# Kernel optimization log

Hardware: AMD Instinct MI355X
Metric: run time of the kernel (lower is better)

The kernel has to match this reference:

```python
import jax, jax.numpy as jnp
import numpy as np

T, D = 1024, 1024            # tokens, model dim
E, K = 16, 4                 # routed experts, top-k
G, TG = 4, 2                 # expert groups, limited (top) groups
INTER = 512                  # moe_inter_dim
SHARED_INTER = 2 * INTER     # n_shared_experts * moe_inter_dim
ROUTE_SCALE = 2.5
STD = 0.02


def setup_inputs() -> dict:
    key = jax.random.key(0)
    ks = jax.random.split(key, 9)
    return {
        "x": jax.random.normal(ks[0], (T, D), jnp.float32),
        "token_mask": jnp.ones((T,), jnp.bool_),
        "gate_w": jax.random.normal(ks[1], (E, D), jnp.float32) * STD,
        "gate_bias": jnp.zeros((E,), jnp.float32),  # e_score_correction_bias (zero-init)
        "gate_projs": jax.random.normal(ks[2], (E, INTER, D), jnp.float32) * STD,
        "up_projs": jax.random.normal(ks[3], (E, INTER, D), jnp.float32) * STD,
        "down_projs": jax.random.normal(ks[4], (E, D, INTER), jnp.float32) * STD,
        "shared_gate": jax.random.normal(ks[5], (SHARED_INTER, D), jnp.float32) * STD,
        "shared_up": jax.random.normal(ks[6], (SHARED_INTER, D), jnp.float32) * STD,
        "shared_down": jax.random.normal(ks[7], (D, SHARED_INTER), jnp.float32) * STD,
    }


def _route(x, gate_w, gate_bias):
    # sigmoid scoring with e_score_correction_bias + group-limited top-k (DeepSeek-V3 style)
    scores = jax.nn.sigmoid(x @ gate_w.T)                      # [T, E]
    s = (scores + gate_bias).reshape(T, G, E // G)             # bias-corrected, grouped
    group_scores = jax.lax.top_k(s, 2)[0].sum(-1)              # [T, G] sum of top-2 per group
    gidx = jax.lax.top_k(group_scores, TG)[1]                  # [T, TG]
    gmask = jax.nn.one_hot(gidx, G, dtype=s.dtype).sum(1)      # [T, G] selected-group mask
    masked = (s * gmask[:, :, None]).reshape(T, E)
    idx = jax.lax.top_k(masked, K)[1]                          # [T, K] expert indices
    w = jnp.take_along_axis(scores, idx, axis=1)               # gather original (unbiased) scores
    w = w / w.sum(-1, keepdims=True) * ROUTE_SCALE             # sigmoid renorm + route scale
    return w.astype(x.dtype), idx


def reference(x, token_mask, gate_w, gate_bias, gate_projs, up_projs,
              down_projs, shared_gate, shared_up, shared_down):
    w, idx = _route(x, gate_w, gate_bias)
    # dense combine weights [T, E]: combine[t, e] = sum_k w[t, k] * (idx[t, k] == e)
    combine = (jax.nn.one_hot(idx, E, dtype=x.dtype) * w[..., None]).sum(1)

    def body(acc, p):
        gp, up, dp, c = p                                      # per-expert SwiGLU
        inter = jax.nn.silu(x @ gp.T) * (x @ up.T)             # [T, INTER]
        return acc + c[:, None] * (inter @ dp.T), None

    routed, _ = jax.lax.scan(
        body, jnp.zeros_like(x), (gate_projs, up_projs, down_projs, combine.T))
    shared = (jax.nn.silu(x @ shared_gate.T) * (x @ shared_up.T)) @ shared_down.T
    return routed + shared
```

## Files before the change

### kernel.cpp

```cpp
#include <hip/hip_runtime.h>
#include <stdint.h>

#define TTOK 1024
#define DMODEL 1024
#define NEXP 16
#define TOPK 4
#define INTER 512
#define NSHI 1024
#define RSCALE 2.5f

typedef __bf16 bf16;
typedef __bf16 bf16x8 __attribute__((ext_vector_type(8)));
typedef __bf16 bf16x4 __attribute__((ext_vector_type(4)));
typedef float f32x4 __attribute__((ext_vector_type(4)));

#define APLANE 2064
#define BPLANE 1040

#define OFF_GP 0L
#define OFF_UP 8388608L
#define OFF_DP 16777216L
#define OFF_SG 25165824L
#define OFF_SU 26214400L
#define OFF_SD 27262976L
#define WTOT   28311552L

#define LGKM_BAR()                                            \
  do {                                                        \
    asm volatile("s_waitcnt lgkmcnt(0)" ::: "memory");        \
    __builtin_amdgcn_s_barrier();                             \
  } while (0)

__global__ __launch_bounds__(256)
void convert_kernel(const float* __restrict__ s0, const float* __restrict__ s1,
                    const float* __restrict__ s2, const float* __restrict__ s3,
                    const float* __restrict__ s4, const float* __restrict__ s5,
                    bf16* __restrict__ dst) {
  const long i = (long)blockIdx.x * 256 + threadIdx.x;
  const float* src;
  long local;
  if (i < 2097152)      { src = s0; local = i; }
  else if (i < 4194304) { src = s1; local = i - 2097152; }
  else if (i < 6291456) { src = s2; local = i - 4194304; }
  else if (i < 6553600) { src = s3; local = i - 6291456; }
  else if (i < 6815744) { src = s4; local = i - 6553600; }
  else                  { src = s5; local = i - 6815744; }
  const float4 v = ((const float4*)src)[local];
  bf16x4 o;
  o.x = (bf16)v.x; o.y = (bf16)v.y; o.z = (bf16)v.z; o.w = (bf16)v.w;
  ((bf16x4*)dst)[i] = o;
}

__global__ __launch_bounds__(256)
void scores_kernel(const float* __restrict__ x, const float* __restrict__ gw,
                   float* __restrict__ scores, bf16* __restrict__ xbf) {
  __shared__ float gws[16 * 1024];
  const int tid = threadIdx.x;
  const float4* gw4 = (const float4*)gw;
#pragma unroll
  for (int i0 = 0; i0 < 4096; i0 += 256) {
    const int i = i0 + tid;
    const int e = i >> 8;
    const int dq = (i & 255) << 2;
    const int dd = (dq + 4 * e) & 1023;
    ((float4*)gws)[(e << 8) + (dd >> 2)] = gw4[i];
  }
  {
    const long xb = (long)blockIdx.x * 1024;
#pragma unroll
    for (int p = 0; p < 4; ++p) {
      const long j = xb + p * 256 + tid;
      const float4 v = ((const float4*)x)[j];
      bf16x4 o;
      o.x = (bf16)v.x; o.y = (bf16)v.y; o.z = (bf16)v.z; o.w = (bf16)v.w;
      ((bf16x4*)xbf)[j] = o;
    }
  }
  __syncthreads();
  const int kq = tid >> 6;
  const int lane = tid & 63;
  const int tl = lane >> 4;
  const int e = lane & 15;
  const long token = (long)blockIdx.x * 4 + tl;
  float acc = 0.f;
  const int dbase = kq * 256;
#pragma unroll 8
  for (int i = 0; i < 256; i += 4) {
    const int d = dbase + i;
    const float4 xv = *(const float4*)&x[token * DMODEL + d];
    const float4 wv = *(const float4*)&gws[(e << 10) + ((d + 4 * e) & 1023)];
    acc += xv.x * wv.x + xv.y * wv.y + xv.z * wv.z + xv.w * wv.w;
  }
  __syncthreads();
  gws[kq * 64 + lane] = acc;
  __syncthreads();
  if (kq == 0) {
    const float s = gws[lane] + gws[64 + lane] + gws[128 + lane] + gws[192 + lane];
    scores[token * 16 + e] = s;
  }
}

__global__ __launch_bounds__(256)
void topk_kernel(const float* __restrict__ scores, const float* __restrict__ gb,
                 int* __restrict__ tokIdx, float* __restrict__ tokW,
                 int* __restrict__ counts) {
  __shared__ int h[NEXP];
  const int tid = threadIdx.x;
  if (tid < NEXP) h[tid] = 0;
  __syncthreads();
  const int t = blockIdx.x * 256 + tid;
  float sc[NEXP], s[NEXP];
#pragma unroll
  for (int e = 0; e < NEXP; ++e) {
    const float l = scores[t * NEXP + e];
    sc[e] = 1.f / (1.f + expf(-l));
    s[e] = sc[e] + gb[e];
  }
  float gsc[4];
#pragma unroll
  for (int g = 0; g < 4; ++g) {
    const float a = s[4 * g], b = s[4 * g + 1], c = s[4 * g + 2], d = s[4 * g + 3];
    gsc[g] = fmaxf(fmaxf(fmaxf(a + b, a + c), fmaxf(a + d, b + c)),
                   fmaxf(b + d, c + d));
  }
  int g0 = 0;
  for (int g = 1; g < 4; ++g) if (gsc[g] > gsc[g0]) g0 = g;
  int g1 = (g0 == 0) ? 1 : 0;
  for (int g = 0; g < 4; ++g) if (g != g0 && gsc[g] > gsc[g1]) g1 = g;
  float m[NEXP];
#pragma unroll
  for (int e = 0; e < NEXP; ++e) {
    const int g = e >> 2;
    m[e] = (g == g0 || g == g1) ? s[e] : -1.f;
  }
  int idx[TOPK]; float wv[TOPK]; float wsum = 0.f;
  for (int k = 0; k < TOPK; ++k) {
    int am = 0; float best = m[0];
    for (int e2 = 1; e2 < NEXP; ++e2)
      if (m[e2] > best) { best = m[e2]; am = e2; }
    idx[k] = am; wv[k] = sc[am]; wsum += sc[am]; m[am] = -2.f;
  }
  const float scl = RSCALE / wsum;
  for (int k = 0; k < TOPK; ++k) {
    tokIdx[t * TOPK + k] = idx[k];
    tokW[t * TOPK + k] = wv[k] * scl;
    atomicAdd(&h[idx[k]], 1);
  }
  __syncthreads();
  if (tid < NEXP) atomicAdd(&counts[tid], h[tid]);
}

__global__ void plan_kernel(const int* __restrict__ counts, int* __restrict__ offs,
                            int* __restrict__ cursors, int* __restrict__ tileE,
                            int* __restrict__ tileR, int* __restrict__ tileCnt) {
  if (threadIdx.x == 0) {
    int acc = 0;
    for (int e = 0; e < NEXP; ++e) { offs[e] = acc; cursors[e] = acc; acc += counts[e]; }
    offs[NEXP] = acc;
    int tc = 0;
    for (int e = 0; e < NEXP; ++e)
      for (int r = offs[e]; r < offs[e + 1]; r += 128) { tileE[tc] = e; tileR[tc] = r; ++tc; }
    for (int r = 0; r < TTOK; r += 128) { tileE[tc] = NEXP; tileR[tc] = r; ++tc; }
    tileCnt[0] = tc;
  }
}

__global__ __launch_bounds__(256)
void fill_kernel(const int* __restrict__ tokIdx, int* __restrict__ cursors,
                 int* __restrict__ slotTok, int* __restrict__ tokSlot) {
  __shared__ int h[NEXP], base[NEXP];
  const int tid = threadIdx.x;
  if (tid < NEXP) h[tid] = 0;
  __syncthreads();
  const int t = blockIdx.x * 256 + tid;
  int myE[TOPK], myR[TOPK];
#pragma unroll
  for (int k = 0; k < TOPK; ++k) {
    myE[k] = tokIdx[t * TOPK + k];
    myR[k] = atomicAdd(&h[myE[k]], 1);
  }
  __syncthreads();
  if (tid < NEXP) base[tid] = atomicAdd(&cursors[tid], h[tid]);
  __syncthreads();
#pragma unroll
  for (int k = 0; k < TOPK; ++k) {
    const int slot = base[myE[k]] + myR[k];
    slotTok[slot] = t;
    tokSlot[t * TOPK + k] = slot;
  }
}

__global__ __launch_bounds__(256, 2)
void gateup_gemm(const bf16* __restrict__ xbf, const int* __restrict__ slotTok,
                 const int* __restrict__ offs, const int* __restrict__ tileE,
                 const int* __restrict__ tileR, const int* __restrict__ tileCnt,
                 const bf16* __restrict__ wbf,
                 bf16* __restrict__ interR, bf16* __restrict__ interS) {
  const int y = blockIdx.y;
  if (y >= tileCnt[0]) return;
  const int e = tileE[y];
  const bool shd = (e == NEXP);
  const int n0 = blockIdx.x * 64;
  if (!shd && n0 >= INTER) return;
  const int rowStart = tileR[y];
  const int rowEnd = shd ? rowStart + 128 : offs[e + 1];
  const bf16* wgp = shd ? wbf + OFF_SG : wbf + OFF_GP + (long)e * INTER * DMODEL;
  const bf16* wup = shd ? wbf + OFF_SU : wbf + OFF_UP + (long)e * INTER * DMODEL;

  __shared__ __attribute__((aligned(16))) char As[8 * APLANE];
  __shared__ __attribute__((aligned(16))) char Bg[8 * BPLANE];
  __shared__ __attribute__((aligned(16))) char Bu[8 * BPLANE];
  __shared__ int tokS[128];

  const int tid = threadIdx.x;
  if (tid < 128) {
    const int r = rowStart + tid;
    tokS[tid] = shd ? r : slotTok[r < rowEnd ? r : rowStart];
  }
  __syncthreads();

  const int arw = tid >> 3;
  const int aoct = tid & 7;
  const bf16* aSrc[4];
#pragma unroll
  for (int p = 0; p < 4; ++p)
    aSrc[p] = xbf + (long)tokS[p * 32 + arw] * DMODEL + aoct * 8;

  const int bu_ = tid >> 7;
  const int u = tid & 127;
  const int brw = u >> 3;
  const int boct = u & 7;
  const bf16* bSrc = (bu_ ? wup : wgp) + (long)(n0 + brw) * DMODEL + boct * 8;
  char* bDst = bu_ ? Bu : Bg;

  const int lane = tid & 63;
  const int wv = tid >> 6;
  const int q = lane >> 4;
  const int l15 = lane & 15;
  const int wm = (wv >> 1) * 64;
  const int wn = (wv & 1) * 32;

  const f32x4 fz = {0.f, 0.f, 0.f, 0.f};
  f32x4 accG[4][2], accU[4][2];
#pragma unroll
  for (int i = 0; i < 4; ++i)
#pragma unroll
    for (int j = 0; j < 2; ++j) { accG[i][j] = fz; accU[i][j] = fz; }

  bf16x8 av[4];
  bf16x8 bv[4];
#pragma unroll
  for (int p = 0; p < 4; ++p) av[p] = *(const bf16x8*)(aSrc[p]);
#pragma unroll
  for (int p = 0; p < 4; ++p)
    bv[p] = *(const bf16x8*)(bSrc + (long)(p * 16) * DMODEL);

  for (int k0 = 0; k0 < DMODEL; k0 += 64) {
    LGKM_BAR();
#pragma unroll
    for (int p = 0; p < 4; ++p)
      *(bf16x8*)(As + aoct * APLANE + (p * 32 + arw) * 16) = av[p];
#pragma unroll
    for (int p = 0; p < 4; ++p)
      *(bf16x8*)(bDst + boct * BPLANE + (p * 16 + brw) * 16) = bv[p];
    const int kn = k0 + 64;
    if (kn < DMODEL) {
#pragma unroll
      for (int p = 0; p < 4; ++p) av[p] = *(const bf16x8*)(aSrc[p] + kn);
#pragma unroll
      for (int p = 0; p < 4; ++p)
        bv[p] = *(const bf16x8*)(bSrc + (long)(p * 16) * DMODEL + kn);
    }
    LGKM_BAR();
#pragma unroll
    for (int kb = 0; kb < 2; ++kb) {
      bf16x8 aF[4];
#pragma unroll
      for (int mi = 0; mi < 4; ++mi)
        aF[mi] = *(const bf16x8*)(As + (4 * kb + q) * APLANE + (wm + 16 * mi + l15) * 16);
#pragma unroll
      for (int ni = 0; ni < 2; ++ni) {
        const int br = wn + 16 * ni + l15;
        const bf16x8 gF = *(const bf16x8*)(Bg + (4 * kb + q) * BPLANE + br * 16);
        const bf16x8 uF = *(const bf16x8*)(Bu + (4 * kb + q) * BPLANE + br * 16);
#pragma unroll
        for (int mi = 0; mi < 4; ++mi) {
          accG[mi][ni] = __builtin_amdgcn_mfma_f32_16x16x32_bf16(aF[mi], gF, accG[mi][ni], 0, 0, 0);
          accU[mi][ni] = __builtin_amdgcn_mfma_f32_16x16x32_bf16(aF[mi], uF, accU[mi][ni], 0, 0, 0);
        }
      }
    }
  }

  bf16* outI = shd ? interS : interR;
  const int ldI = shd ? NSHI : INTER;
#pragma unroll
  for (int mi = 0; mi < 4; ++mi)
#pragma unroll
    for (int r = 0; r < 4; ++r) {
      const int rowLoc = wm + 16 * mi + q * 4 + r;
      const int row = rowStart + rowLoc;
      if (row < rowEnd) {
#pragma unroll
        for (int ni = 0; ni < 2; ++ni) {
          const float gg = accG[mi][ni][r];
          const float uu = accU[mi][ni][r];
          const float sv = gg / (1.f + __expf(-gg)) * uu;
          outI[(long)row * ldI + (n0 + wn + 16 * ni + l15)] = (bf16)sv;
        }
      }
    }
}

__global__ __launch_bounds__(256, 2)
void down_gemm(const bf16* __restrict__ interR, const bf16* __restrict__ interS,
               const int* __restrict__ offs, const int* __restrict__ tileE,
               const int* __restrict__ tileR, const int* __restrict__ tileCnt,
               const bf16* __restrict__ wbf,
               float* __restrict__ dsR, float* __restrict__ dsS) {
  const int y = blockIdx.y;
  if (y >= tileCnt[0]) return;
  const int e = tileE[y];
  const bool shd = (e == NEXP);
  const int n0 = blockIdx.x * 64;
  const int rowStart = tileR[y];
  const int rowEnd = shd ? rowStart + 128 : offs[e + 1];
  const int Kd = shd ? NSHI : INTER;
  const bf16* A = shd ? interS : interR;
  const bf16* wd = shd ? wbf + OFF_SD : wbf + OFF_DP + (long)e * DMODEL * INTER;

  __shared__ __attribute__((aligned(16))) char As[8 * APLANE];
  __shared__ __attribute__((aligned(16))) char Bs[8 * BPLANE];

  const int tid = threadIdx.x;
  const int arw = tid >> 3;
  const int aoct = tid & 7;
  const bf16* aSrc[4];
#pragma unroll
  for (int p = 0; p < 4; ++p)
    aSrc[p] = A + (long)(rowStart + p * 32 + arw) * Kd + aoct * 8;

  const int brw = tid >> 3;
  const int boct = tid & 7;
  const bf16* bSrc = wd + (long)(n0 + brw) * Kd + boct * 8;

  const int lane = tid & 63;
  const int wv = tid >> 6;
  const int q = lane >> 4;
  const int l15 = lane & 15;
  const int wm = (wv >> 1) * 64;
  const int wn = (wv & 1) * 32;

  const f32x4 fz = {0.f, 0.f, 0.f, 0.f};
  f32x4 acc[4][2];
#pragma unroll
  for (int i = 0; i < 4; ++i)
#pragma unroll
    for (int j = 0; j < 2; ++j) acc[i][j] = fz;

  bf16x8 av[4];
  bf16x8 bv[2];
#pragma unroll
  for (int p = 0; p < 4; ++p) av[p] = *(const bf16x8*)(aSrc[p]);
#pragma unroll
  for (int p = 0; p < 2; ++p)
    bv[p] = *(const bf16x8*)(bSrc + (long)(p * 32) * Kd);

  for (int k0 = 0; k0 < Kd; k0 += 64) {
    LGKM_BAR();
#pragma unroll
    for (int p = 0; p < 4; ++p)
      *(bf16x8*)(As + aoct * APLANE + (p * 32 + arw) * 16) = av[p];
#pragma unroll
    for (int p = 0; p < 2; ++p)
      *(bf16x8*)(Bs + boct * BPLANE + (p * 32 + brw) * 16) = bv[p];
    const int kn = k0 + 64;
    if (kn < Kd) {
#pragma unroll
      for (int p = 0; p < 4; ++p) av[p] = *(const bf16x8*)(aSrc[p] + kn);
#pragma unroll
      for (int p = 0; p < 2; ++p)
        bv[p] = *(const bf16x8*)(bSrc + (long)(p * 32) * Kd + kn);
    }
    LGKM_BAR();
#pragma unroll
    for (int kb = 0; kb < 2; ++kb) {
      bf16x8 aF[4];
#pragma unroll
      for (int mi = 0; mi < 4; ++mi)
        aF[mi] = *(const bf16x8*)(As + (4 * kb + q) * APLANE + (wm + 16 * mi + l15) * 16);
#pragma unroll
      for (int ni = 0; ni < 2; ++ni) {
        const bf16x8 bF = *(const bf16x8*)(Bs + (4 * kb + q) * BPLANE + (wn + 16 * ni + l15) * 16);
#pragma unroll
        for (int mi = 0; mi < 4; ++mi)
          acc[mi][ni] = __builtin_amdgcn_mfma_f32_16x16x32_bf16(aF[mi], bF, acc[mi][ni], 0, 0, 0);
      }
    }
  }

  float* dst = shd ? dsS : dsR;
#pragma unroll
  for (int mi = 0; mi < 4; ++mi)
#pragma unroll
    for (int r = 0; r < 4; ++r) {
      const int rowLoc = wm + 16 * mi + q * 4 + r;
      const int row = rowStart + rowLoc;
      if (row < rowEnd) {
#pragma unroll
        for (int ni = 0; ni < 2; ++ni)
          dst[(long)row * DMODEL + (n0 + wn + 16 * ni + l15)] = acc[mi][ni][r];
      }
    }
}

__global__ __launch_bounds__(256)
void combine_kernel(const float* __restrict__ dsR, const float* __restrict__ dsS,
                    const int* __restrict__ tokSlot, const float* __restrict__ tokW,
                    float* __restrict__ out) {
  const int t = blockIdx.x;
  const int j = threadIdx.x;
  float4 v = ((const float4*)(dsS + (long)t * DMODEL))[j];
#pragma unroll
  for (int k = 0; k < TOPK; ++k) {
    const int s = tokSlot[t * TOPK + k];
    const float w = tokW[t * TOPK + k];
    const float4 r = ((const float4*)(dsR + (long)s * DMODEL))[j];
    v.x += w * r.x; v.y += w * r.y; v.z += w * r.z; v.w += w * r.w;
  }
  ((float4*)(out + (long)t * DMODEL))[j] = v;
}

extern "C" void kernel_launch(void* const* d_in, const int* in_sizes, int n_in,
                              void* d_out, int out_size, void* d_ws, size_t ws_size,
                              hipStream_t stream) {
  const float* x  = (const float*)d_in[0];
  const float* gw = (const float*)d_in[2];
  const float* gb = (const float*)d_in[3];
  const float* gp = (const float*)d_in[4];
  const float* up = (const float*)d_in[5];
  const float* dp = (const float*)d_in[6];
  const float* sg = (const float*)d_in[7];
  const float* su = (const float*)d_in[8];
  const float* sd = (const float*)d_in[9];
  float* out = (float*)d_out;

  char* base = (char*)d_ws;
  size_t off = 0;
  auto alloc = [&](size_t bytes) -> char* {
    off = (off + 255) & ~(size_t)255;
    char* p = base + off;
    off += bytes;
    return p;
  };
  bf16* wbf = (bf16*)alloc((size_t)WTOT * 2);
  bf16* xbf = (bf16*)alloc((size_t)TTOK * DMODEL * 2);
  bf16* interR = (bf16*)alloc((size_t)(TTOK * TOPK + 128) * INTER * 2);
  bf16* interS = (bf16*)alloc((size_t)TTOK * NSHI * 2);
  float* dsR = (float*)alloc((size_t)TTOK * TOPK * DMODEL * 4);
  float* dsS = (float*)alloc((size_t)TTOK * DMODEL * 4);
  float* scores = (float*)alloc((size_t)TTOK * NEXP * 4);
  int* tokIdx = (int*)alloc(TTOK * TOPK * 4);
  float* tokW = (float*)alloc(TTOK * TOPK * 4);
  int* slotTok = (int*)alloc(TTOK * TOPK * 4);
  int* tokSlot = (int*)alloc(TTOK * TOPK * 4);
  int* counts = (int*)alloc(NEXP * 4);
  int* offs = (int*)alloc((NEXP + 1) * 4);
  int* cursors = (int*)alloc(NEXP * 4);
  int* tileE = (int*)alloc(72 * 4);
  int* tileR = (int*)alloc(72 * 4);
  int* tileCnt = (int*)alloc(4);

  hipMemsetAsync(counts, 0, NEXP * 4, stream);

  convert_kernel<<<27648, 256, 0, stream>>>(gp, up, dp, sg, su, sd, wbf);
  scores_kernel<<<TTOK / 4, 256, 0, stream>>>(x, gw, scores, xbf);
  topk_kernel<<<TTOK / 256, 256, 0, stream>>>(scores, gb, tokIdx, tokW, counts);
  plan_kernel<<<1, 64, 0, stream>>>(counts, offs, cursors, tileE, tileR, tileCnt);
  fill_kernel<<<TTOK / 256, 256, 0, stream>>>(tokIdx, cursors, slotTok, tokSlot);

  gateup_gemm<<<dim3(16, 56, 1), 256, 0, stream>>>(
      xbf, slotTok, offs, tileE, tileR, tileCnt, wbf, interR, interS);
  down_gemm<<<dim3(16, 56, 1), 256, 0, stream>>>(
      interR, interS, offs, tileE, tileR, tileCnt, wbf, dsR, dsS);
  combine_kernel<<<TTOK, 256, 0, stream>>>(dsR, dsS, tokSlot, tokW, out);
}
```

Measured before the change: 222.8 us.

## Fuse routing stages into one kernel and widen weight conversion per thread

Merges topk, plan and fill into a single 1024-thread route kernel that uses shared-memory counters and cursors. This removes a memset, two kernel launches and the global atomics between them. The convert kernel now has each thread handle four 8-element chunks with 32-byte loads and 16-byte stores, using far fewer blocks. Slot ordering inside each expert changes, since it now depends on the order of shared atomics, but the result stays correct because tokSlot maps each token back to its slot.

```diff
diff --git a/kernel.cpp b/kernel.cpp
--- a/kernel.cpp
+++ b/kernel.cpp
@@ -31,24 +31,31 @@
     __builtin_amdgcn_s_barrier();                             \
   } while (0)
 
+#define CV_STRIDE 884736L
 __global__ __launch_bounds__(256)
 void convert_kernel(const float* __restrict__ s0, const float* __restrict__ s1,
                     const float* __restrict__ s2, const float* __restrict__ s3,
                     const float* __restrict__ s4, const float* __restrict__ s5,
                     bf16* __restrict__ dst) {
-  const long i = (long)blockIdx.x * 256 + threadIdx.x;
-  const float* src;
-  long local;
-  if (i < 2097152)      { src = s0; local = i; }
-  else if (i < 4194304) { src = s1; local = i - 2097152; }
-  else if (i < 6291456) { src = s2; local = i - 4194304; }
-  else if (i < 6553600) { src = s3; local = i - 6291456; }
-  else if (i < 6815744) { src = s4; local = i - 6553600; }
-  else                  { src = s5; local = i - 6815744; }
-  const float4 v = ((const float4*)src)[local];
-  bf16x4 o;
-  o.x = (bf16)v.x; o.y = (bf16)v.y; o.z = (bf16)v.z; o.w = (bf16)v.w;
-  ((bf16x4*)dst)[i] = o;
+  const long j0 = (long)blockIdx.x * 256 + threadIdx.x;
+#pragma unroll
+  for (int it = 0; it < 4; ++it) {
+    const long j = j0 + (long)it * CV_STRIDE;
+    const float* src;
+    long local;
+    if (j < 1048576L)      { src = s0; local = j; }
+    else if (j < 2097152L) { src = s1; local = j - 1048576L; }
+    else if (j < 3145728L) { src = s2; local = j - 2097152L; }
+    else if (j < 3276800L) { src = s3; local = j - 3145728L; }
+    else if (j < 3407872L) { src = s4; local = j - 3276800L; }
+    else                   { src = s5; local = j - 3407872L; }
+    const float4 a = ((const float4*)src)[local * 2];
+    const float4 b = ((const float4*)src)[local * 2 + 1];
+    bf16x8 o;
+    o[0] = (bf16)a.x; o[1] = (bf16)a.y; o[2] = (bf16)a.z; o[3] = (bf16)a.w;
+    o[4] = (bf16)b.x; o[5] = (bf16)b.y; o[6] = (bf16)b.z; o[7] = (bf16)b.w;
+    ((bf16x8*)dst)[j] = o;
+  }
 }
 
 __global__ __launch_bounds__(256)
@@ -100,15 +107,16 @@
   }
 }
 
-__global__ __launch_bounds__(256)
-void topk_kernel(const float* __restrict__ scores, const float* __restrict__ gb,
-                 int* __restrict__ tokIdx, float* __restrict__ tokW,
-                 int* __restrict__ counts) {
-  __shared__ int h[NEXP];
-  const int tid = threadIdx.x;
-  if (tid < NEXP) h[tid] = 0;
-  __syncthreads();
-  const int t = blockIdx.x * 256 + tid;
+__global__ __launch_bounds__(1024)
+void route_kernel(const float* __restrict__ scores, const float* __restrict__ gb,
+                  float* __restrict__ tokW, int* __restrict__ slotTok,
+                  int* __restrict__ tokSlot, int* __restrict__ offs,
+                  int* __restrict__ tileE, int* __restrict__ tileR,
+                  int* __restrict__ tileCnt) {
+  __shared__ int cnt[NEXP], cur[NEXP];
+  const int t = threadIdx.x;
+  if (t < NEXP) cnt[t] = 0;
+  __syncthreads();
   float sc[NEXP], s[NEXP];
 #pragma unroll
   for (int e = 0; e < NEXP; ++e) {
@@ -140,53 +148,34 @@
       if (m[e2] > best) { best = m[e2]; am = e2; }
     idx[k] = am; wv[k] = sc[am]; wsum += sc[am]; m[am] = -2.f;
   }
-  const float scl = RSCALE / wsum;
-  for (int k = 0; k < TOPK; ++k) {
-    tokIdx[t * TOPK + k] = idx[k];
-    tokW[t * TOPK + k] = wv[k] * scl;
-    atomicAdd(&h[idx[k]], 1);
-  }
-  __syncthreads();
-  if (tid < NEXP) atomicAdd(&counts[tid], h[tid]);
-}
-
-__global__ void plan_kernel(const int* __restrict__ counts, int* __restrict__ offs,
-                            int* __restrict__ cursors, int* __restrict__ tileE,
-                            int* __restrict__ tileR, int* __restrict__ tileCnt) {
-  if (threadIdx.x == 0) {
+#pragma unroll
+  for (int k = 0; k < TOPK; ++k) atomicAdd(&cnt[idx[k]], 1);
+  __syncthreads();
+  if (t == 0) {
     int acc = 0;
-    for (int e = 0; e < NEXP; ++e) { offs[e] = acc; cursors[e] = acc; acc += counts[e]; }
+#pragma unroll
+    for (int e = 0; e < NEXP; ++e) {
+      offs[e] = acc; cur[e] = acc; acc += cnt[e];
+    }
     offs[NEXP] = acc;
     int tc = 0;
-    for (int e = 0; e < NEXP; ++e)
-      for (int r = offs[e]; r < offs[e + 1]; r += 128) { tileE[tc] = e; tileR[tc] = r; ++tc; }
+    int roff = 0;
+    for (int e = 0; e < NEXP; ++e) {
+      const int end = roff + cnt[e];
+      for (int r = roff; r < end; r += 128) { tileE[tc] = e; tileR[tc] = r; ++tc; }
+      roff = end;
+    }
     for (int r = 0; r < TTOK; r += 128) { tileE[tc] = NEXP; tileR[tc] = r; ++tc; }
     tileCnt[0] = tc;
   }
-}
-
-__global__ __launch_bounds__(256)
-void fill_kernel(const int* __restrict__ tokIdx, int* __restrict__ cursors,
-                 int* __restrict__ slotTok, int* __restrict__ tokSlot) {
-  __shared__ int h[NEXP], base[NEXP];
-  const int tid = threadIdx.x;
-  if (tid < NEXP) h[tid] = 0;
-  __syncthreads();
-  const int t = blockIdx.x * 256 + tid;
-  int myE[TOPK], myR[TOPK];
+  __syncthreads();
+  const float scl = RSCALE / wsum;
 #pragma unroll
   for (int k = 0; k < TOPK; ++k) {
-    myE[k] = tokIdx[t * TOPK + k];
-    myR[k] = atomicAdd(&h[myE[k]], 1);
-  }
-  __syncthreads();
-  if (tid < NEXP) base[tid] = atomicAdd(&cursors[tid], h[tid]);
-  __syncthreads();
-#pragma unroll
-  for (int k = 0; k < TOPK; ++k) {
-    const int slot = base[myE[k]] + myR[k];
+    const int slot = atomicAdd(&cur[idx[k]], 1);
     slotTok[slot] = t;
     tokSlot[t * TOPK + k] = slot;
+    tokW[t * TOPK + k] = wv[k] * scl;
   }
 }
 
@@ -460,24 +449,18 @@
   float* dsR = (float*)alloc((size_t)TTOK * TOPK * DMODEL * 4);
   float* dsS = (float*)alloc((size_t)TTOK * DMODEL * 4);
   float* scores = (float*)alloc((size_t)TTOK * NEXP * 4);
-  int* tokIdx = (int*)alloc(TTOK * TOPK * 4);
   float* tokW = (float*)alloc(TTOK * TOPK * 4);
   int* slotTok = (int*)alloc(TTOK * TOPK * 4);
   int* tokSlot = (int*)alloc(TTOK * TOPK * 4);
-  int* counts = (int*)alloc(NEXP * 4);
   int* offs = (int*)alloc((NEXP + 1) * 4);
-  int* cursors = (int*)alloc(NEXP * 4);
   int* tileE = (int*)alloc(72 * 4);
   int* tileR = (int*)alloc(72 * 4);
   int* tileCnt = (int*)alloc(4);
 
-  hipMemsetAsync(counts, 0, NEXP * 4, stream);
-
-  convert_kernel<<<27648, 256, 0, stream>>>(gp, up, dp, sg, su, sd, wbf);
+  convert_kernel<<<3456, 256, 0, stream>>>(gp, up, dp, sg, su, sd, wbf);
   scores_kernel<<<TTOK / 4, 256, 0, stream>>>(x, gw, scores, xbf);
-  topk_kernel<<<TTOK / 256, 256, 0, stream>>>(scores, gb, tokIdx, tokW, counts);
-  plan_kernel<<<1, 64, 0, stream>>>(counts, offs, cursors, tileE, tileR, tileCnt);
-  fill_kernel<<<TTOK / 256, 256, 0, stream>>>(tokIdx, cursors, slotTok, tokSlot);
+  route_kernel<<<1, 1024, 0, stream>>>(scores, gb, tokW, slotTok, tokSlot,
+                                       offs, tileE, tileR, tileCnt);
 
   gateup_gemm<<<dim3(16, 56, 1), 256, 0, stream>>>(
       xbf, slotTok, offs, tileE, tileR, tileCnt, wbf, interR, interS);
```

After: 225.0 us. About the same (+1.0%).
